# Kernel optimization log

Measured on AMD Instinct MI355X. Metric: run time of the kernel, lower is better.

The kernel has to match this reference:

```python
import jax, jax.numpy as jnp
import numpy as np

S, B, H, K = 4096, 1, 2048, 2  # seq_len, batch (forced to 1 by the view()), hidden_dim, conv kernel
EMBED = K * K                  # embed_dim must equal kernel_size**2
THRESHOLD = 0.0


def setup_inputs() -> dict:
    key = jax.random.key(0)
    k0, k1, k2 = jax.random.split(key, 3)
    inputs = jax.random.normal(k0, (S, B, EMBED), dtype=jnp.float32)
    # ConvFilter params: Conv2d(1,1,K) on a KxK patch == dot with flattened kernel + bias
    conv_w = jax.random.normal(k1, (EMBED,), dtype=jnp.float32) * 0.5
    conv_b = jnp.zeros((1,), dtype=jnp.float32)
    # Four gate Linears (1+H -> H) stacked column-wise into one (1+H, 4H) matmul
    # order: forget | input | update | output  (same math as 4 separate nn.Linear)
    w_gates = (jax.random.normal(k2, (1 + H, 4 * H), dtype=jnp.float32)
               / np.sqrt(1.0 + H)).astype(jnp.float32)
    b_gates = jnp.zeros((4 * H,), dtype=jnp.float32)
    return {"inputs": inputs, "conv_w": conv_w, "conv_b": conv_b,
            "w_gates": w_gates, "b_gates": b_gates}


def reference(inputs, conv_w, conv_b, w_gates, b_gates):
    S_, B_, _ = inputs.shape
    H_ = w_gates.shape[1] // 4

    # Conv preprocess (vectorized over all timesteps): each (K,K) token patch
    # -> scalar sigmoid(conv(x) - threshold), then mean over the per-step batch
    # (batch==1, so the mean is the value itself, matching torch's .mean()).
    conv_scalar = jax.nn.sigmoid(inputs @ conv_w + conv_b[0] - THRESHOLD)  # (S, B)
    conv_scalar = jnp.mean(conv_scalar, axis=1, keepdims=True)             # (S, 1)
    conv_out = jnp.broadcast_to(conv_scalar[:, :, None], (S_, B_, 1))      # (S, B, 1)

    hx0 = jnp.zeros((B_, H_), dtype=inputs.dtype)
    cx0 = jnp.zeros((B_, H_), dtype=inputs.dtype)

    def step(carry, c_t):
        hx, cx = carry
        combined = jnp.concatenate([c_t, hx], axis=1)        # (B, 1+H)
        gates = combined @ w_gates + b_gates                  # (B, 4H) fused 4-gate GEMM
        f, i, g, o = jnp.split(gates, 4, axis=1)
        f = jax.nn.sigmoid(f)
        i = jax.nn.sigmoid(i)
        g = jnp.tanh(g)
        o = jax.nn.sigmoid(o)
        cx = f * cx + i * g
        hx = o * jnp.tanh(cx)
        return (hx, cx), hx

    (hx, cx), stacked = jax.lax.scan(step, (hx0, cx0), conv_out)
    return stacked, hx, cx
```

## Files before the change

kernel.cpp:

```cpp
#include <hip/hip_runtime.h>
#include <math.h>

#define S_LEN 4096
#define HID   2048
#define NBLK  256
#define NTHR  512

typedef unsigned int       u32;
typedef unsigned long long u64;
typedef unsigned u32x4 __attribute__((ext_vector_type(4)));


__device__ __forceinline__ float fast_sigmoid(float x) {
    float e = __builtin_amdgcn_exp2f(-1.44269504f * x);
    return __builtin_amdgcn_rcpf(1.0f + e);
}

__global__ __launch_bounds__(NTHR, 2)
void qlstm_persistent(const float* __restrict__ inp,
                      const float* __restrict__ conv_w,
                      const float* __restrict__ conv_b,
                      const float* __restrict__ Wg,
                      const float* __restrict__ bg,
                      float* __restrict__ out,
                      float* __restrict__ ws)
{
    const int b   = blockIdx.x;
    const int tid = threadIdx.x;
    const int l   = tid & 63;
    const int wv  = tid >> 6;

    u32* tbl = (u32*)ws;

    __shared__ __align__(16) float hx_lds[HID];
    __shared__ __align__(16) float conv_lds[S_LEN];
    __shared__ float gates_lds[32];
    __shared__ float colw0[32];
    __shared__ float colb[32];

    {
        const float cw0 = conv_w[0], cw1 = conv_w[1], cw2 = conv_w[2], cw3 = conv_w[3];
        const float cb  = conv_b[0];
        for (int g = tid; g < S_LEN; g += NTHR) {
            float4 x = ((const float4*)inp)[g];
            float v = x.x*cw0 + x.y*cw1 + x.z*cw2 + x.w*cw3 + cb;
            conv_lds[g] = fast_sigmoid(v);
        }
    }
    ((float4*)hx_lds)[tid] = make_float4(0.f, 0.f, 0.f, 0.f);

    int jcol[4];
    #pragma unroll
    for (int c = 0; c < 4; ++c) {
        int cgi  = 4*wv + c;
        int gate = cgi >> 3;
        int mi   = cgi & 7;
        jcol[c]  = (gate << 11) + (b * 8 + mi);
    }
    if (l == 0) {
        #pragma unroll
        for (int c = 0; c < 4; ++c) {
            int cgi = 4*wv + c;
            colw0[cgi] = Wg[jcol[c]];
            colb[cgi]  = bg[jcol[c]];
        }
    }

    float wreg[4][32];
    #pragma unroll
    for (int j = 0; j < 8; ++j)
        #pragma unroll
        for (int r = 0; r < 4; ++r) {
            const float* rowp = Wg + (size_t)(1 + 4*l + 256*j + r) * 8192;
            #pragma unroll
            for (int c = 0; c < 4; ++c)
                wreg[c][4*j + r] = rowp[jcol[c]];
        }

    float cx = 0.0f;
    const int m_out = b * 8 + tid;

    const u32* poll_base = tbl + (tid >> 1) * 16 + (tid & 1) * 4;
    u32* pub_base = tbl + b * 16 + tid;

    for (int t = 0; t < S_LEN; ++t) {
        if (t) {
            const u32 want = ((u32)(t + 1) & 3u) ^ 2u;
            const u32* pp = poll_base + ((t & 1) << 3);
            u32x4 q;
            u32 miss;
            do {
                asm volatile("global_load_dwordx4 %0, %1, off sc0 sc1\n\t"
                             "s_waitcnt vmcnt(0)"
                             : "=v"(q) : "v"(pp) : "memory");
                miss = ((q[0] ^ want) & 3u) | ((q[1] ^ want) & 3u)
                     | ((q[2] ^ want) & 3u) | ((q[3] ^ want) & 3u);
            } while (miss);
            u32x4 st;
            st[0] = q[0] & ~3u; st[1] = q[1] & ~3u;
            st[2] = q[2] & ~3u; st[3] = q[3] & ~3u;
            ((u32x4*)hx_lds)[tid] = st;
        }
        __syncthreads();

        const float4* hl = (const float4*)hx_lds;
        float acc0 = 0.f, acc1 = 0.f, acc2 = 0.f, acc3 = 0.f;
        #pragma unroll
        for (int j = 0; j < 8; ++j) {
            float4 h = hl[l + 64*j];
            acc0 = fmaf(h.x, wreg[0][4*j+0], acc0);
            acc1 = fmaf(h.x, wreg[1][4*j+0], acc1);
            acc2 = fmaf(h.x, wreg[2][4*j+0], acc2);
            acc3 = fmaf(h.x, wreg[3][4*j+0], acc3);
            acc0 = fmaf(h.y, wreg[0][4*j+1], acc0);
            acc1 = fmaf(h.y, wreg[1][4*j+1], acc1);
            acc2 = fmaf(h.y, wreg[2][4*j+1], acc2);
            acc3 = fmaf(h.y, wreg[3][4*j+1], acc3);
            acc0 = fmaf(h.z, wreg[0][4*j+2], acc0);
            acc1 = fmaf(h.z, wreg[1][4*j+2], acc1);
            acc2 = fmaf(h.z, wreg[2][4*j+2], acc2);
            acc3 = fmaf(h.z, wreg[3][4*j+2], acc3);
            acc0 = fmaf(h.w, wreg[0][4*j+3], acc0);
            acc1 = fmaf(h.w, wreg[1][4*j+3], acc1);
            acc2 = fmaf(h.w, wreg[2][4*j+3], acc2);
            acc3 = fmaf(h.w, wreg[3][4*j+3], acc3);
        }
        #pragma unroll
        for (int off = 32; off; off >>= 1) {
            acc0 += __shfl_down(acc0, off, 64);
            acc1 += __shfl_down(acc1, off, 64);
            acc2 += __shfl_down(acc2, off, 64);
            acc3 += __shfl_down(acc3, off, 64);
        }
        if (l == 0) {
            gates_lds[4*wv + 0] = acc0;
            gates_lds[4*wv + 1] = acc1;
            gates_lds[4*wv + 2] = acc2;
            gates_lds[4*wv + 3] = acc3;
        }
        __syncthreads();

        if (wv == 0) __builtin_amdgcn_s_setprio(1);
        if (tid < 8) {
            float ct = conv_lds[t];
            float fg = gates_lds[tid]      + ct*colw0[tid]      + colb[tid];
            float ig = gates_lds[8 + tid]  + ct*colw0[8 + tid]  + colb[8 + tid];
            float gg = gates_lds[16 + tid] + ct*colw0[16 + tid] + colb[16 + tid];
            float og = gates_lds[24 + tid] + ct*colw0[24 + tid] + colb[24 + tid];
            float f  = fast_sigmoid(fg);
            float ii = fast_sigmoid(ig);
            float gv = 2.0f * fast_sigmoid(2.0f * gg) - 1.0f;
            float o  = fast_sigmoid(og);
            cx = f * cx + ii * gv;
            float hx = o * (2.0f * fast_sigmoid(2.0f * cx) - 1.0f);
            u32 word = (__float_as_uint(hx) & ~3u) | (((u32)(t + 2) & 3u) ^ 2u);
            __hip_atomic_store(pub_base + (((t + 1) & 1) << 3), word,
                               __ATOMIC_RELAXED, __HIP_MEMORY_SCOPE_AGENT);
            out[(size_t)t * HID + m_out] = hx;
            if (t == S_LEN - 1) {
                out[(size_t)S_LEN * HID + m_out]       = hx;
                out[(size_t)S_LEN * HID + HID + m_out] = cx;
            }
        }
        if (wv == 0) __builtin_amdgcn_s_setprio(0);
    }
}

extern "C" void kernel_launch(void* const* d_in, const int* in_sizes, int n_in,
                              void* d_out, int out_size, void* d_ws, size_t ws_size,
                              hipStream_t stream) {
    const float* inp    = (const float*)d_in[0];
    const float* conv_w = (const float*)d_in[1];
    const float* conv_b = (const float*)d_in[2];
    const float* Wg     = (const float*)d_in[3];
    const float* bg     = (const float*)d_in[4];
    float* out = (float*)d_out;
    float* ws  = (float*)d_ws;

    void* args[] = {(void*)&inp, (void*)&conv_w, (void*)&conv_b,
                    (void*)&Wg, (void*)&bg, (void*)&out, (void*)&ws};
    hipLaunchCooperativeKernel((void*)qlstm_persistent,
                               dim3(NBLK), dim3(NTHR), args, 0, stream);
}
```

Measured before the change: 11.45 ms.

## Add dedicated poller wavefront with per-group LDS flags replacing block barriers

Adds a ninth wavefront that polls the global hidden-state table for each timestep and copies the data into a double-buffered LDS hx array. It signals per-chunk readiness through LDS counters so the compute wavefronts can begin their partial dot products on chunks as they arrive. Both __syncthreads per step are replaced by flag-based handoffs: compute waves publish their gate partials with release stores, and wave 0 spins on those flags before the nonlinearity. This is meant to overlap the cross-block polling with the FMAs and remove full-block barrier latency. In exchange it adds LDS spin loops and more complex memory ordering, and drops occupancy to one block per CU.

Result: slower. 23.31 ms (+103.5%).

```diff
diff --git a/kernel.cpp b/kernel.cpp
--- a/kernel.cpp
+++ b/kernel.cpp
@@ -4,7 +4,7 @@
 #define S_LEN 4096
 #define HID   2048
 #define NBLK  256
-#define NTHR  512
+#define NTHR  576
 
 typedef unsigned int       u32;
 typedef unsigned long long u64;
@@ -16,7 +16,7 @@
     return __builtin_amdgcn_rcpf(1.0f + e);
 }
 
-__global__ __launch_bounds__(NTHR, 2)
+__global__ __launch_bounds__(NTHR, 1)
 void qlstm_persistent(const float* __restrict__ inp,
                       const float* __restrict__ conv_w,
                       const float* __restrict__ conv_b,
@@ -32,11 +32,13 @@
 
     u32* tbl = (u32*)ws;
 
-    __shared__ __align__(16) float hx_lds[HID];
+    __shared__ __align__(16) float hx_lds[2][HID];
     __shared__ __align__(16) float conv_lds[S_LEN];
-    __shared__ float gates_lds[32];
+    __shared__ float gates_lds[2][32];
     __shared__ float colw0[32];
     __shared__ float colb[32];
+    __shared__ u32 rdyc[2][8];
+    __shared__ u32 gep[2][8];
 
     {
         const float cw0 = conv_w[0], cw1 = conv_w[1], cw2 = conv_w[2], cw3 = conv_w[3];
@@ -47,122 +49,193 @@
             conv_lds[g] = fast_sigmoid(v);
         }
     }
-    ((float4*)hx_lds)[tid] = make_float4(0.f, 0.f, 0.f, 0.f);
-
-    int jcol[4];
-    #pragma unroll
-    for (int c = 0; c < 4; ++c) {
-        int cgi  = 4*wv + c;
-        int gate = cgi >> 3;
-        int mi   = cgi & 7;
-        jcol[c]  = (gate << 11) + (b * 8 + mi);
-    }
-    if (l == 0) {
+    if (tid < 512) ((float4*)hx_lds[0])[tid] = make_float4(0.f, 0.f, 0.f, 0.f);
+    if (tid < 16) {
+        rdyc[tid >> 3][tid & 7] = 0u;
+        gep[tid >> 3][tid & 7]  = 0xFFFFFFFFu;
+    }
+
+    float wreg[4][32];
+    if (wv < 8) {
+        int jcol[4];
         #pragma unroll
         for (int c = 0; c < 4; ++c) {
-            int cgi = 4*wv + c;
-            colw0[cgi] = Wg[jcol[c]];
-            colb[cgi]  = bg[jcol[c]];
-        }
-    }
-
-    float wreg[4][32];
-    #pragma unroll
-    for (int j = 0; j < 8; ++j)
+            int cgi  = 4*wv + c;
+            int gate = cgi >> 3;
+            int mi   = cgi & 7;
+            jcol[c]  = (gate << 11) + (b * 8 + mi);
+        }
+        if (l == 0) {
+            #pragma unroll
+            for (int c = 0; c < 4; ++c) {
+                int cgi = 4*wv + c;
+                colw0[cgi] = Wg[jcol[c]];
+                colb[cgi]  = bg[jcol[c]];
+            }
+        }
         #pragma unroll
-        for (int r = 0; r < 4; ++r) {
-            const float* rowp = Wg + (size_t)(1 + 4*l + 256*j + r) * 8192;
-            #pragma unroll
-            for (int c = 0; c < 4; ++c)
-                wreg[c][4*j + r] = rowp[jcol[c]];
-        }
-
-    float cx = 0.0f;
-    const int m_out = b * 8 + tid;
-
-    const u32* poll_base = tbl + (tid >> 1) * 16 + (tid & 1) * 4;
-    u32* pub_base = tbl + b * 16 + tid;
-
-    for (int t = 0; t < S_LEN; ++t) {
-        if (t) {
-            const u32 want = ((u32)(t + 1) & 3u) ^ 2u;
-            const u32* pp = poll_base + ((t & 1) << 3);
-            u32x4 q;
-            u32 miss;
+        for (int j = 0; j < 8; ++j)
+            #pragma unroll
+            for (int r = 0; r < 4; ++r) {
+                const float* rowp = Wg + (size_t)(1 + 4*l + 256*j + r) * 8192;
+                #pragma unroll
+                for (int c = 0; c < 4; ++c)
+                    wreg[c][4*j + r] = rowp[jcol[c]];
+            }
+    }
+
+    __syncthreads();
+
+    if (wv == 8) {
+        __builtin_amdgcn_s_setprio(1);
+        const u32* lane_base = tbl + ((l >> 1) << 4) + ((l & 1) << 2);
+        for (int T = 1; T < S_LEN; ++T) {
+            const int pT = T & 1;
+            const u32 want = ((u32)(T + 1) & 3u) ^ 2u;
+            const u32* ap = lane_base + (pT << 3);
+            const u32 *a0 = ap,        *a1 = ap + 512,  *a2 = ap + 1024, *a3 = ap + 1536,
+                      *a4 = ap + 2048, *a5 = ap + 2560, *a6 = ap + 3072, *a7 = ap + 3584;
+            u32x4* dst = (u32x4*)hx_lds[pT];
+            u32 bits = 0, prev = 0, ldone = 0;
             do {
-                asm volatile("global_load_dwordx4 %0, %1, off sc0 sc1\n\t"
-                             "s_waitcnt vmcnt(0)"
-                             : "=v"(q) : "v"(pp) : "memory");
-                miss = ((q[0] ^ want) & 3u) | ((q[1] ^ want) & 3u)
-                     | ((q[2] ^ want) & 3u) | ((q[3] ^ want) & 3u);
-            } while (miss);
-            u32x4 st;
-            st[0] = q[0] & ~3u; st[1] = q[1] & ~3u;
-            st[2] = q[2] & ~3u; st[3] = q[3] & ~3u;
-            ((u32x4*)hx_lds)[tid] = st;
-        }
-        __syncthreads();
-
-        const float4* hl = (const float4*)hx_lds;
-        float acc0 = 0.f, acc1 = 0.f, acc2 = 0.f, acc3 = 0.f;
-        #pragma unroll
-        for (int j = 0; j < 8; ++j) {
-            float4 h = hl[l + 64*j];
-            acc0 = fmaf(h.x, wreg[0][4*j+0], acc0);
-            acc1 = fmaf(h.x, wreg[1][4*j+0], acc1);
-            acc2 = fmaf(h.x, wreg[2][4*j+0], acc2);
-            acc3 = fmaf(h.x, wreg[3][4*j+0], acc3);
-            acc0 = fmaf(h.y, wreg[0][4*j+1], acc0);
-            acc1 = fmaf(h.y, wreg[1][4*j+1], acc1);
-            acc2 = fmaf(h.y, wreg[2][4*j+1], acc2);
-            acc3 = fmaf(h.y, wreg[3][4*j+1], acc3);
-            acc0 = fmaf(h.z, wreg[0][4*j+2], acc0);
-            acc1 = fmaf(h.z, wreg[1][4*j+2], acc1);
-            acc2 = fmaf(h.z, wreg[2][4*j+2], acc2);
-            acc3 = fmaf(h.z, wreg[3][4*j+2], acc3);
-            acc0 = fmaf(h.w, wreg[0][4*j+3], acc0);
-            acc1 = fmaf(h.w, wreg[1][4*j+3], acc1);
-            acc2 = fmaf(h.w, wreg[2][4*j+3], acc2);
-            acc3 = fmaf(h.w, wreg[3][4*j+3], acc3);
-        }
-        #pragma unroll
-        for (int off = 32; off; off >>= 1) {
-            acc0 += __shfl_down(acc0, off, 64);
-            acc1 += __shfl_down(acc1, off, 64);
-            acc2 += __shfl_down(acc2, off, 64);
-            acc3 += __shfl_down(acc3, off, 64);
-        }
-        if (l == 0) {
-            gates_lds[4*wv + 0] = acc0;
-            gates_lds[4*wv + 1] = acc1;
-            gates_lds[4*wv + 2] = acc2;
-            gates_lds[4*wv + 3] = acc3;
-        }
-        __syncthreads();
-
-        if (wv == 0) __builtin_amdgcn_s_setprio(1);
-        if (tid < 8) {
-            float ct = conv_lds[t];
-            float fg = gates_lds[tid]      + ct*colw0[tid]      + colb[tid];
-            float ig = gates_lds[8 + tid]  + ct*colw0[8 + tid]  + colb[8 + tid];
-            float gg = gates_lds[16 + tid] + ct*colw0[16 + tid] + colb[16 + tid];
-            float og = gates_lds[24 + tid] + ct*colw0[24 + tid] + colb[24 + tid];
-            float f  = fast_sigmoid(fg);
-            float ii = fast_sigmoid(ig);
-            float gv = 2.0f * fast_sigmoid(2.0f * gg) - 1.0f;
-            float o  = fast_sigmoid(og);
-            cx = f * cx + ii * gv;
-            float hx = o * (2.0f * fast_sigmoid(2.0f * cx) - 1.0f);
-            u32 word = (__float_as_uint(hx) & ~3u) | (((u32)(t + 2) & 3u) ^ 2u);
-            __hip_atomic_store(pub_base + (((t + 1) & 1) << 3), word,
-                               __ATOMIC_RELAXED, __HIP_MEMORY_SCOPE_AGENT);
-            out[(size_t)t * HID + m_out] = hx;
-            if (t == S_LEN - 1) {
-                out[(size_t)S_LEN * HID + m_out]       = hx;
-                out[(size_t)S_LEN * HID + HID + m_out] = cx;
-            }
-        }
-        if (wv == 0) __builtin_amdgcn_s_setprio(0);
+                u32x4 q0, q1, q2, q3, q4, q5, q6, q7;
+                asm volatile(
+                    "global_load_dwordx4 %0, %8,  off sc0 sc1\n\t"
+                    "global_load_dwordx4 %1, %9,  off sc0 sc1\n\t"
+                    "global_load_dwordx4 %2, %10, off sc0 sc1\n\t"
+                    "global_load_dwordx4 %3, %11, off sc0 sc1\n\t"
+                    "global_load_dwordx4 %4, %12, off sc0 sc1\n\t"
+                    "global_load_dwordx4 %5, %13, off sc0 sc1\n\t"
+                    "global_load_dwordx4 %6, %14, off sc0 sc1\n\t"
+                    "global_load_dwordx4 %7, %15, off sc0 sc1\n\t"
+                    "s_waitcnt vmcnt(0)"
+                    : "=&v"(q0), "=&v"(q1), "=&v"(q2), "=&v"(q3),
+                      "=&v"(q4), "=&v"(q5), "=&v"(q6), "=&v"(q7)
+                    : "v"(a0), "v"(a1), "v"(a2), "v"(a3),
+                      "v"(a4), "v"(a5), "v"(a6), "v"(a7)
+                    : "memory");
+                #define GRP(g, qq)                                               \
+                    if (!(bits & (1u << g))) {                                   \
+                        bool ok = ((qq[0] & 3u) == want) && ((qq[1] & 3u) == want) \
+                               && ((qq[2] & 3u) == want) && ((qq[3] & 3u) == want); \
+                        if (ok && !(ldone & (1u << g))) {                        \
+                            u32x4 st;                                            \
+                            st[0] = qq[0] & ~3u; st[1] = qq[1] & ~3u;            \
+                            st[2] = qq[2] & ~3u; st[3] = qq[3] & ~3u;            \
+                            dst[(g << 6) + l] = st;                              \
+                            ldone |= 1u << g;                                    \
+                        }                                                        \
+                        if (__ballot(ok) == ~0ull) bits |= 1u << g;              \
+                    }
+                GRP(0, q0) GRP(1, q1) GRP(2, q2) GRP(3, q3)
+                GRP(4, q4) GRP(5, q5) GRP(6, q6) GRP(7, q7)
+                #undef GRP
+                u32 newbits = bits & ~prev;
+                if (l == 0 && newbits) {
+                    #pragma unroll
+                    for (int g = 0; g < 8; ++g)
+                        if (newbits & (1u << g))
+                            __hip_atomic_store(&rdyc[pT][g], (u32)T,
+                                               __ATOMIC_RELEASE,
+                                               __HIP_MEMORY_SCOPE_WORKGROUP);
+                }
+                prev = bits;
+            } while (bits != 0xFFu);
+        }
+    } else {
+        float cx = 0.0f;
+        const int m_out = b * 8 + l;
+        for (int t = 0; t < S_LEN; ++t) {
+            const int p = t & 1;
+            const u32 ut = (u32)t;
+            const float4* hl = (const float4*)hx_lds[p];
+
+            u32 mready = 0;
+            #pragma unroll
+            for (int j = 0; j < 8; ++j)
+                mready |= (__hip_atomic_load(&rdyc[p][j], __ATOMIC_RELAXED,
+                                             __HIP_MEMORY_SCOPE_WORKGROUP) >= ut)
+                          ? (1u << j) : 0u;
+            __threadfence_block();
+
+            float acc0 = 0.f, acc1 = 0.f, acc2 = 0.f, acc3 = 0.f;
+            #pragma unroll
+            for (int j = 0; j < 8; ++j) {
+                if (!(mready & (1u << j))) {
+                    u32 r;
+                    do { r = __hip_atomic_load(&rdyc[p][j], __ATOMIC_RELAXED,
+                                               __HIP_MEMORY_SCOPE_WORKGROUP); }
+                    while (r < ut);
+                    __threadfence_block();
+                }
+                float4 h = hl[l + 64*j];
+                acc0 = fmaf(h.x, wreg[0][4*j+0], acc0);
+                acc1 = fmaf(h.x, wreg[1][4*j+0], acc1);
+                acc2 = fmaf(h.x, wreg[2][4*j+0], acc2);
+                acc3 = fmaf(h.x, wreg[3][4*j+0], acc3);
+                acc0 = fmaf(h.y, wreg[0][4*j+1], acc0);
+                acc1 = fmaf(h.y, wreg[1][4*j+1], acc1);
+                acc2 = fmaf(h.y, wreg[2][4*j+1], acc2);
+                acc3 = fmaf(h.y, wreg[3][4*j+1], acc3);
+                acc0 = fmaf(h.z, wreg[0][4*j+2], acc0);
+                acc1 = fmaf(h.z, wreg[1][4*j+2], acc1);
+                acc2 = fmaf(h.z, wreg[2][4*j+2], acc2);
+                acc3 = fmaf(h.z, wreg[3][4*j+2], acc3);
+                acc0 = fmaf(h.w, wreg[0][4*j+3], acc0);
+                acc1 = fmaf(h.w, wreg[1][4*j+3], acc1);
+                acc2 = fmaf(h.w, wreg[2][4*j+3], acc2);
+                acc3 = fmaf(h.w, wreg[3][4*j+3], acc3);
+            }
+            #pragma unroll
+            for (int off = 32; off; off >>= 1) {
+                acc0 += __shfl_down(acc0, off, 64);
+                acc1 += __shfl_down(acc1, off, 64);
+                acc2 += __shfl_down(acc2, off, 64);
+                acc3 += __shfl_down(acc3, off, 64);
+            }
+            if (l == 0) {
+                gates_lds[p][4*wv + 0] = acc0;
+                gates_lds[p][4*wv + 1] = acc1;
+                gates_lds[p][4*wv + 2] = acc2;
+                gates_lds[p][4*wv + 3] = acc3;
+                __hip_atomic_store(&gep[p][wv], ut, __ATOMIC_RELEASE,
+                                   __HIP_MEMORY_SCOPE_WORKGROUP);
+            }
+
+            if (wv == 0) {
+                u32 g;
+                do { g = __hip_atomic_load(&gep[p][l & 7], __ATOMIC_ACQUIRE,
+                                           __HIP_MEMORY_SCOPE_WORKGROUP); }
+                while (!__all(g == ut));
+                __builtin_amdgcn_s_setprio(1);
+                if (l < 8) {
+                    float ct = conv_lds[t];
+                    float fg = gates_lds[p][l]      + ct*colw0[l]      + colb[l];
+                    float ig = gates_lds[p][8 + l]  + ct*colw0[8 + l]  + colb[8 + l];
+                    float gg = gates_lds[p][16 + l] + ct*colw0[16 + l] + colb[16 + l];
+                    float og = gates_lds[p][24 + l] + ct*colw0[24 + l] + colb[24 + l];
+                    float f  = fast_sigmoid(fg);
+                    float ii = fast_sigmoid(ig);
+                    float gv = 2.0f * fast_sigmoid(2.0f * gg) - 1.0f;
+                    float o  = fast_sigmoid(og);
+                    cx = f * cx + ii * gv;
+                    float hx = o * (2.0f * fast_sigmoid(2.0f * cx) - 1.0f);
+                    if (t < S_LEN - 1) {
+                        u32 word = (__float_as_uint(hx) & ~3u)
+                                 | (((u32)(t + 2) & 3u) ^ 2u);
+                        __hip_atomic_store(tbl + b*16 + (((t + 1) & 1) << 3) + l,
+                                           word, __ATOMIC_RELAXED,
+                                           __HIP_MEMORY_SCOPE_AGENT);
+                    }
+                    out[(size_t)t * HID + m_out] = hx;
+                    if (t == S_LEN - 1) {
+                        out[(size_t)S_LEN * HID + m_out]       = hx;
+                        out[(size_t)S_LEN * HID + HID + m_out] = cx;
+                    }
+                }
+                __builtin_amdgcn_s_setprio(0);
+            }
+        }
     }
 }
 
```

## Replace block barriers with per-wave LDS flag handoff and double-buffered hx

Applied to the files above, without the earlier changes.

Removes both __syncthreads per timestep. Each wave now publishes its polled slice of hx into a double-buffered LDS array and marks a per-wave step counter. Consumers spin on the counter for each slice before using it. Gate partials are signalled through a second flag array that wave 0 polls before doing the cell update. This lets waves start their dot products as soon as individual slices arrive rather than waiting for the whole block, at the cost of LDS spin loops and subtle memory-ordering risk. The launch-bound hint also changes to amdgpu_waves_per_eu(2,2), and the final step no longer publishes hx.

New measurement: 12.79 ms. 11.6% more time.

```diff
diff --git a/kernel.cpp b/kernel.cpp
--- a/kernel.cpp
+++ b/kernel.cpp
@@ -16,7 +16,8 @@
     return __builtin_amdgcn_rcpf(1.0f + e);
 }
 
-__global__ __launch_bounds__(NTHR, 2)
+__global__ __launch_bounds__(NTHR)
+__attribute__((amdgpu_waves_per_eu(2, 2)))
 void qlstm_persistent(const float* __restrict__ inp,
                       const float* __restrict__ conv_w,
                       const float* __restrict__ conv_b,
@@ -32,11 +33,13 @@
 
     u32* tbl = (u32*)ws;
 
-    __shared__ __align__(16) float hx_lds[HID];
+    __shared__ __align__(16) float hx_lds[2][HID];
     __shared__ __align__(16) float conv_lds[S_LEN];
-    __shared__ float gates_lds[32];
+    __shared__ float gates_lds[2][32];
     __shared__ float colw0[32];
     __shared__ float colb[32];
+    __shared__ u32 ck[2][8];
+    __shared__ u32 gep[2][8];
 
     {
         const float cw0 = conv_w[0], cw1 = conv_w[1], cw2 = conv_w[2], cw3 = conv_w[3];
@@ -47,7 +50,13 @@
             conv_lds[g] = fast_sigmoid(v);
         }
     }
-    ((float4*)hx_lds)[tid] = make_float4(0.f, 0.f, 0.f, 0.f);
+    ((float4*)hx_lds[0])[tid] = make_float4(0.f, 0.f, 0.f, 0.f);
+    if (tid < 8) {
+        ck[0][tid]  = 1u;
+        ck[1][tid]  = 0u;
+        gep[0][tid] = 0u;
+        gep[1][tid] = 0u;
+    }
 
     int jcol[4];
     #pragma unroll
@@ -83,10 +92,15 @@
     const u32* poll_base = tbl + (tid >> 1) * 16 + (tid & 1) * 4;
     u32* pub_base = tbl + b * 16 + tid;
 
+    __syncthreads();
+
     for (int t = 0; t < S_LEN; ++t) {
+        const int p   = t & 1;
+        const u32 stp = (u32)(t + 1);
+
         if (t) {
-            const u32 want = ((u32)(t + 1) & 3u) ^ 2u;
-            const u32* pp = poll_base + ((t & 1) << 3);
+            const u32 want = (stp & 3u) ^ 2u;
+            const u32* pp = poll_base + (p << 3);
             u32x4 q;
             u32 miss;
             do {
@@ -99,14 +113,20 @@
             u32x4 st;
             st[0] = q[0] & ~3u; st[1] = q[1] & ~3u;
             st[2] = q[2] & ~3u; st[3] = q[3] & ~3u;
-            ((u32x4*)hx_lds)[tid] = st;
-        }
-        __syncthreads();
-
-        const float4* hl = (const float4*)hx_lds;
+            ((u32x4*)hx_lds[p])[tid] = st;
+            if (l == 0)
+                __hip_atomic_store(&ck[p][wv], stp, __ATOMIC_RELEASE,
+                                   __HIP_MEMORY_SCOPE_WORKGROUP);
+        }
+
+        const float4* hl = (const float4*)hx_lds[p];
         float acc0 = 0.f, acc1 = 0.f, acc2 = 0.f, acc3 = 0.f;
         #pragma unroll
         for (int j = 0; j < 8; ++j) {
+            if (t && j != wv) {
+                while (__hip_atomic_load(&ck[p][j], __ATOMIC_ACQUIRE,
+                                         __HIP_MEMORY_SCOPE_WORKGROUP) < stp) {}
+            }
             float4 h = hl[l + 64*j];
             acc0 = fmaf(h.x, wreg[0][4*j+0], acc0);
             acc1 = fmaf(h.x, wreg[1][4*j+0], acc1);
@@ -133,36 +153,47 @@
             acc3 += __shfl_down(acc3, off, 64);
         }
         if (l == 0) {
-            gates_lds[4*wv + 0] = acc0;
-            gates_lds[4*wv + 1] = acc1;
-            gates_lds[4*wv + 2] = acc2;
-            gates_lds[4*wv + 3] = acc3;
-        }
-        __syncthreads();
-
-        if (wv == 0) __builtin_amdgcn_s_setprio(1);
-        if (tid < 8) {
-            float ct = conv_lds[t];
-            float fg = gates_lds[tid]      + ct*colw0[tid]      + colb[tid];
-            float ig = gates_lds[8 + tid]  + ct*colw0[8 + tid]  + colb[8 + tid];
-            float gg = gates_lds[16 + tid] + ct*colw0[16 + tid] + colb[16 + tid];
-            float og = gates_lds[24 + tid] + ct*colw0[24 + tid] + colb[24 + tid];
-            float f  = fast_sigmoid(fg);
-            float ii = fast_sigmoid(ig);
-            float gv = 2.0f * fast_sigmoid(2.0f * gg) - 1.0f;
-            float o  = fast_sigmoid(og);
-            cx = f * cx + ii * gv;
-            float hx = o * (2.0f * fast_sigmoid(2.0f * cx) - 1.0f);
-            u32 word = (__float_as_uint(hx) & ~3u) | (((u32)(t + 2) & 3u) ^ 2u);
-            __hip_atomic_store(pub_base + (((t + 1) & 1) << 3), word,
-                               __ATOMIC_RELAXED, __HIP_MEMORY_SCOPE_AGENT);
-            out[(size_t)t * HID + m_out] = hx;
-            if (t == S_LEN - 1) {
-                out[(size_t)S_LEN * HID + m_out]       = hx;
-                out[(size_t)S_LEN * HID + HID + m_out] = cx;
+            gates_lds[p][4*wv + 0] = acc0;
+            gates_lds[p][4*wv + 1] = acc1;
+            gates_lds[p][4*wv + 2] = acc2;
+            gates_lds[p][4*wv + 3] = acc3;
+            __hip_atomic_store(&gep[p][wv], stp, __ATOMIC_RELEASE,
+                               __HIP_MEMORY_SCOPE_WORKGROUP);
+        }
+
+        if (wv == 0) {
+            u32 g;
+            do {
+                g = __hip_atomic_load(&gep[p][l & 7], __ATOMIC_ACQUIRE,
+                                      __HIP_MEMORY_SCOPE_WORKGROUP);
+            } while (!__all(g >= stp));
+            __builtin_amdgcn_s_setprio(1);
+            if (l < 8) {
+                float ct = conv_lds[t];
+                float fg = gates_lds[p][tid]      + ct*colw0[tid]      + colb[tid];
+                float ig = gates_lds[p][8 + tid]  + ct*colw0[8 + tid]  + colb[8 + tid];
+                float gg = gates_lds[p][16 + tid] + ct*colw0[16 + tid] + colb[16 + tid];
+                float og = gates_lds[p][24 + tid] + ct*colw0[24 + tid] + colb[24 + tid];
+                float f  = fast_sigmoid(fg);
+                float ii = fast_sigmoid(ig);
+                float gv = 2.0f * fast_sigmoid(2.0f * gg) - 1.0f;
+                float o  = fast_sigmoid(og);
+                cx = f * cx + ii * gv;
+                float hx = o * (2.0f * fast_sigmoid(2.0f * cx) - 1.0f);
+                if (t < S_LEN - 1) {
+                    u32 word = (__float_as_uint(hx) & ~3u)
+                             | (((u32)(t + 2) & 3u) ^ 2u);
+                    __hip_atomic_store(pub_base + (((t + 1) & 1) << 3), word,
+                                       __ATOMIC_RELAXED, __HIP_MEMORY_SCOPE_AGENT);
+                }
+                out[(size_t)t * HID + m_out] = hx;
+                if (t == S_LEN - 1) {
+                    out[(size_t)S_LEN * HID + m_out]       = hx;
+                    out[(size_t)S_LEN * HID + HID + m_out] = cx;
+                }
             }
-        }
-        if (wv == 0) __builtin_amdgcn_s_setprio(0);
+            __builtin_amdgcn_s_setprio(0);
+        }
     }
 }
 
```
